# Kernel optimization log

Measured on AMD Instinct MI355X. Metric: run time of the kernel, lower is better.

The kernel has to match this reference:

```python
import jax, jax.numpy as jnp
import numpy as np

PRIMES = (2, 3, 5, 7, 11, 13, 17, 19, 23, 29)
TEMP = 1000.0  # softmax_temperature
B, S = 32, 2048

def _templates(p):
    # circle template for residue r: (cos(2*pi*r/p), sin(2*pi*r/p)) -> [p, 2]
    ang = 2.0 * np.pi * np.arange(p) / p
    return jnp.asarray(np.stack([np.cos(ang), np.sin(ang)], axis=-1).astype(np.float32))

def _mul_onehot(p):
    # onehot[a, b, (a*b) % p] = 1 -> [p, p, p]
    t = (np.arange(p)[:, None] * np.arange(p)[None, :]) % p
    return jnp.asarray((t[..., None] == np.arange(p)).astype(np.float32))

TEMPLATES = [_templates(p) for p in PRIMES]
MUL_OH = [_mul_onehot(p) for p in PRIMES]

def setup_inputs() -> dict:
    key = jax.random.key(0)
    k1, k2 = jax.random.split(key)
    m = len(PRIMES)
    return {
        "a_circle": jax.random.normal(k1, (B, S, m, 2), dtype=jnp.float32),
        "b_circle": jax.random.normal(k2, (B, S, m, 2), dtype=jnp.float32),
    }

def _circle_add(a, b):
    # complex multiply: angles add -> (a + b) mod p on the circle
    ca, sa = a[..., 0], a[..., 1]
    cb, sb = b[..., 0], b[..., 1]
    return jnp.stack([ca * cb - sa * sb, sa * cb + ca * sb], axis=-1)

def _circle_sub(a, b):
    # a - b = a + conj(b): negate sin of b
    b_conj = jnp.stack([b[..., 0], -b[..., 1]], axis=-1)
    return _circle_add(a, b_conj)

def _decode_soft(c_i, tmpl):
    # c_i: [B, S, 2], tmpl: [p, 2] -> soft one-hot over residues [B, S, p]
    sim = jnp.einsum('bsd,pd->bsp', c_i, tmpl)
    return jax.nn.softmax(TEMP * sim, axis=-1)

def _circle_mul(a, b):
    outs = []
    for i, p in enumerate(PRIMES):
        tmpl = TEMPLATES[i]
        a_soft = _decode_soft(a[:, :, i, :], tmpl)
        b_soft = _decode_soft(b[:, :, i, :], tmpl)
        # outer product of soft residues contracted with mul table
        dist = jnp.einsum('bsi,bsj,ijk->bsk', a_soft, b_soft, MUL_OH[i])
        outs.append(dist @ tmpl)  # re-encode to circle: [B, S, 2]
    return jnp.stack(outs, axis=2)  # [B, S, m, 2]

def reference(a_circle, b_circle):
    add = _circle_add(a_circle, b_circle)
    sub = _circle_sub(a_circle, b_circle)
    mul = _circle_mul(a_circle, b_circle)
    return jnp.stack([add, sub, mul], axis=0)  # [3, B, S, m, 2]
```

## Files before the change

### kernel.cpp

```cpp
#include <hip/hip_runtime.h>


#define TEMP_LOG2E 1442.6950408889634f

constexpr double PI_D = 3.14159265358979323846264338327950288;

constexpr double tay_cos(double x) {
    double x2 = x * x, term = 1.0, sum = 1.0;
    for (int k = 1; k <= 15; ++k) { term *= -x2 / double((2 * k - 1) * (2 * k)); sum += term; }
    return sum;
}
constexpr double tay_sin(double x) {
    double x2 = x * x, term = x, sum = x;
    for (int k = 1; k <= 15; ++k) { term *= -x2 / double((2 * k) * (2 * k + 1)); sum += term; }
    return sum;
}
constexpr double ang_red(int r, int P) {
    double x = 2.0 * PI_D * double(r) / double(P);
    return (x > PI_D) ? x - 2.0 * PI_D : x;
}

template <int P> struct TabS { float c[P]; float s[P]; };
template <int P>
constexpr TabS<P> make_tabs() {
    TabS<P> t{};
    for (int r = 0; r < P; ++r) {
        t.c[r] = (float)(double(TEMP_LOG2E) * tay_cos(ang_red(r, P)));
        t.s[r] = (float)(double(TEMP_LOG2E) * tay_sin(ang_red(r, P)));
    }
    return t;
}
template <int P> struct TabE { float c[P / 2 + 1]; float s[P / 2 + 1]; };
template <int P>
constexpr TabE<P> make_tabe() {
    TabE<P> t{};
    for (int k = 0; k <= P / 2; ++k) {
        t.c[k] = (float)tay_cos(ang_red(k, P));
        t.s[k] = (float)tay_sin(ang_red(k, P));
    }
    return t;
}

template <int P>
__device__ __forceinline__ void mul_prime(float ca, float sa, float cb, float sb,
                                          float& oc, float& os) {
    static_assert(P % 2 == 1, "generic path requires odd P");
    constexpr int H = (P - 1) / 2;
    constexpr TabS<P> T = make_tabs<P>();
    constexpr TabE<P> E = make_tabe<P>();

    float ma = -1e30f, mb = -1e30f;
#pragma unroll
    for (int r = 0; r < P; ++r) {
        ma = fmaxf(ma, ca * T.c[r] + sa * T.s[r]);
        mb = fmaxf(mb, cb * T.c[r] + sb * T.s[r]);
    }

    float eb0 = __builtin_amdgcn_exp2f(cb * T.c[0] - mb);
    float Sb = eb0;
    float ub[H], vb[H];
#pragma unroll
    for (int j = 1; j <= H; ++j) {
        float e1 = __builtin_amdgcn_exp2f(cb * T.c[j] + sb * T.s[j] - mb);
        float e2 = __builtin_amdgcn_exp2f(cb * T.c[P - j] + sb * T.s[P - j] - mb);
        Sb += e1 + e2;
        ub[j - 1] = e1 + e2;
        vb[j - 1] = e1 - e2;
    }

    float A[H], Bacc[H];
#pragma unroll
    for (int k = 0; k < H; ++k) { A[k] = 0.f; Bacc[k] = 0.f; }

    float ea0 = __builtin_amdgcn_exp2f(ca * T.c[0] - ma);
    float Sa = ea0;
#pragma unroll
    for (int i = 1; i <= H; ++i) {
        float f1 = __builtin_amdgcn_exp2f(ca * T.c[i] + sa * T.s[i] - ma);
        float f2 = __builtin_amdgcn_exp2f(ca * T.c[P - i] + sa * T.s[P - i] - ma);
        Sa += f1 + f2;
        const float ua = f1 + f2, va = f1 - f2;
#pragma unroll
        for (int j = 1; j <= H; ++j) {
            const int k0 = (i * j) % P;
            const int kr = (k0 <= H) ? k0 : P - k0;
            A[kr - 1] = fmaf(ua, ub[j - 1], A[kr - 1]);
            if (k0 <= H) Bacc[kr - 1] = fmaf(va,  vb[j - 1], Bacc[kr - 1]);
            else         Bacc[kr - 1] = fmaf(-va, vb[j - 1], Bacc[kr - 1]);
        }
    }

    const float W0 = ea0 * Sb + eb0 * (Sa - ea0);

    float accC = W0, accS = 0.f;
#pragma unroll
    for (int k = 1; k <= H; ++k) {
        accC = fmaf(A[k - 1],    E.c[k], accC);
        accS = fmaf(Bacc[k - 1], E.s[k], accS);
    }
    const float inv = 1.0f / (Sa * Sb);
    oc = accC * inv;
    os = accS * inv;
}

template <>
__device__ __forceinline__ void mul_prime<2>(float ca, float sa, float cb, float sb,
                                             float& oc, float& os) {
    const float ka = ca * TEMP_LOG2E, kb = cb * TEMP_LOG2E;
    const float ma = fabsf(ka), mb = fabsf(kb);
    const float ea0 = __builtin_amdgcn_exp2f(ka - ma);
    const float ea1 = __builtin_amdgcn_exp2f(-ka - ma);
    const float eb0 = __builtin_amdgcn_exp2f(kb - mb);
    const float eb1 = __builtin_amdgcn_exp2f(-kb - mb);
    const float Sa = ea0 + ea1, Sb = eb0 + eb1;
    const float W0 = ea0 * Sb + eb0 * Sa - ea0 * eb0;
    const float W1 = ea1 * eb1;
    oc = (W0 - W1) / (Sa * Sb);
    os = 0.f;
}

__global__ __launch_bounds__(640, 2) void arith_kernel(const float* __restrict__ a,
                                                       const float* __restrict__ b,
                                                       float* __restrict__ out,
                                                       int n_pairs) {
    __shared__ float2 t0[64 * 11], t1[64 * 11];
    __shared__ float2 o2[64 * 11];

    const int t = threadIdx.x;
    const int pr = t / 10, of = t - pr * 10;
    const int li = pr * 11 + of;
    const int gf = blockIdx.x * 640 + t;
    const int planef2 = n_pairs * 10;
    float2* o = (float2*)out;

    {
        const float2 av = ((const float2*)a)[gf];
        const float2 bv = ((const float2*)b)[gf];
        t0[li] = av;
        t1[li] = bv;
        const float pcc = av.x * bv.x, pss = av.y * bv.y;
        const float psc = av.y * bv.x, pcs = av.x * bv.y;
        o[gf]           = make_float2(pcc - pss, psc + pcs);
        o[planef2 + gf] = make_float2(pcc + pss, psc - pcs);
    }
    __syncthreads();

    {
        const int lane = t & 63;
        const int pi = t >> 6;
        const int lc = lane * 11 + pi;
        const float2 av = t0[lc];
        const float2 bv = t1[lc];
        float oc, os;
        switch (pi) {
            case 0: mul_prime<2>(av.x, av.y, bv.x, bv.y, oc, os); break;
            case 1: mul_prime<3>(av.x, av.y, bv.x, bv.y, oc, os); break;
            case 2: mul_prime<5>(av.x, av.y, bv.x, bv.y, oc, os); break;
            case 3: mul_prime<7>(av.x, av.y, bv.x, bv.y, oc, os); break;
            case 4: mul_prime<11>(av.x, av.y, bv.x, bv.y, oc, os); break;
            case 5: mul_prime<13>(av.x, av.y, bv.x, bv.y, oc, os); break;
            case 6: mul_prime<17>(av.x, av.y, bv.x, bv.y, oc, os); break;
            case 7: mul_prime<19>(av.x, av.y, bv.x, bv.y, oc, os); break;
            case 8: mul_prime<23>(av.x, av.y, bv.x, bv.y, oc, os); break;
            default: mul_prime<29>(av.x, av.y, bv.x, bv.y, oc, os); break;
        }
        o2[lc] = make_float2(oc, os);
    }
    __syncthreads();

    o[2 * planef2 + gf] = o2[li];
}

extern "C" void kernel_launch(void* const* d_in, const int* in_sizes, int n_in,
                              void* d_out, int out_size, void* d_ws, size_t ws_size,
                              hipStream_t stream) {
    const float* a = (const float*)d_in[0];
    const float* b = (const float*)d_in[1];
    float* out = (float*)d_out;
    const int n_pairs = in_sizes[0] / 20;
    const int n_groups = n_pairs / 64;

    dim3 block(640);
    dim3 grid(n_groups);
    arith_kernel<<<grid, block, 0, stream>>>(a, b, out, n_pairs);
}
```

Measured before the change: 74.34 us.

## Rebalance prime work across waves with 256-thread blocks of 128 rows

Replaces the one-wave-per-prime mapping, where the wave handling p=29 dominated block latency, with 4 waves per block covering 128 rows. Two waves each run primes {29,17,13,2} and the other two run {23,19,11,7,5,3}, which evens out the cost per wave. Loads and add/sub stores now loop 5 times per thread. The intent is to remove the load imbalance caused by the largest-prime wave. In exchange, each thread carries more serialized work and uses more registers, and occupancy may change.

```diff
diff --git a/kernel.cpp b/kernel.cpp
--- a/kernel.cpp
+++ b/kernel.cpp
@@ -119,56 +119,70 @@
     os = 0.f;
 }
 
-__global__ __launch_bounds__(640, 2) void arith_kernel(const float* __restrict__ a,
+__global__ __launch_bounds__(256, 2) void arith_kernel(const float* __restrict__ a,
                                                        const float* __restrict__ b,
                                                        float* __restrict__ out,
                                                        int n_pairs) {
-    __shared__ float2 t0[64 * 11], t1[64 * 11];
-    __shared__ float2 o2[64 * 11];
+    __shared__ float2 ta[128 * 11], tb[128 * 11], om[128 * 11];
 
     const int t = threadIdx.x;
-    const int pr = t / 10, of = t - pr * 10;
-    const int li = pr * 11 + of;
-    const int gf = blockIdx.x * 640 + t;
+    const int gbase = blockIdx.x * 1280;
     const int planef2 = n_pairs * 10;
     float2* o = (float2*)out;
 
-    {
-        const float2 av = ((const float2*)a)[gf];
-        const float2 bv = ((const float2*)b)[gf];
-        t0[li] = av;
-        t1[li] = bv;
+#pragma unroll
+    for (int it = 0; it < 5; ++it) {
+        const int idx = it * 256 + t;
+        const int pr = idx / 10, of = idx - pr * 10;
+        const int sl = pr * 11 + of;
+        const float2 av = ((const float2*)a)[gbase + idx];
+        const float2 bv = ((const float2*)b)[gbase + idx];
+        ta[sl] = av;
+        tb[sl] = bv;
         const float pcc = av.x * bv.x, pss = av.y * bv.y;
         const float psc = av.y * bv.x, pcs = av.x * bv.y;
-        o[gf]           = make_float2(pcc - pss, psc + pcs);
-        o[planef2 + gf] = make_float2(pcc + pss, psc - pcs);
+        o[gbase + idx]            = make_float2(pcc - pss, psc + pcs);
+        o[planef2 + gbase + idx]  = make_float2(pcc + pss, psc - pcs);
     }
     __syncthreads();
 
     {
         const int lane = t & 63;
-        const int pi = t >> 6;
-        const int lc = lane * 11 + pi;
-        const float2 av = t0[lc];
-        const float2 bv = t1[lc];
-        float oc, os;
-        switch (pi) {
-            case 0: mul_prime<2>(av.x, av.y, bv.x, bv.y, oc, os); break;
-            case 1: mul_prime<3>(av.x, av.y, bv.x, bv.y, oc, os); break;
-            case 2: mul_prime<5>(av.x, av.y, bv.x, bv.y, oc, os); break;
-            case 3: mul_prime<7>(av.x, av.y, bv.x, bv.y, oc, os); break;
-            case 4: mul_prime<11>(av.x, av.y, bv.x, bv.y, oc, os); break;
-            case 5: mul_prime<13>(av.x, av.y, bv.x, bv.y, oc, os); break;
-            case 6: mul_prime<17>(av.x, av.y, bv.x, bv.y, oc, os); break;
-            case 7: mul_prime<19>(av.x, av.y, bv.x, bv.y, oc, os); break;
-            case 8: mul_prime<23>(av.x, av.y, bv.x, bv.y, oc, os); break;
-            default: mul_prime<29>(av.x, av.y, bv.x, bv.y, oc, os); break;
+        const int row = ((t >> 6) & 1) * 64 + lane;
+        const int rb = row * 11;
+
+#define DO_PRIME(P, OFI)                                                     \
+        {                                                                    \
+            const float2 av = ta[rb + (OFI)];                                \
+            const float2 bv = tb[rb + (OFI)];                                \
+            float oc, os;                                                    \
+            mul_prime<P>(av.x, av.y, bv.x, bv.y, oc, os);                    \
+            om[rb + (OFI)] = make_float2(oc, os);                            \
         }
-        o2[lc] = make_float2(oc, os);
+
+        if (t < 128) {
+            DO_PRIME(29, 9)
+            DO_PRIME(17, 6)
+            DO_PRIME(13, 5)
+            DO_PRIME(2, 0)
+        } else {
+            DO_PRIME(23, 8)
+            DO_PRIME(19, 7)
+            DO_PRIME(11, 4)
+            DO_PRIME(7, 3)
+            DO_PRIME(5, 2)
+            DO_PRIME(3, 1)
+        }
+#undef DO_PRIME
     }
     __syncthreads();
 
-    o[2 * planef2 + gf] = o2[li];
+#pragma unroll
+    for (int it = 0; it < 5; ++it) {
+        const int idx = it * 256 + t;
+        const int pr = idx / 10, of = idx - pr * 10;
+        o[2 * planef2 + gbase + idx] = om[pr * 11 + of];
+    }
 }
 
 extern "C" void kernel_launch(void* const* d_in, const int* in_sizes, int n_in,
@@ -178,9 +192,9 @@
     const float* b = (const float*)d_in[1];
     float* out = (float*)d_out;
     const int n_pairs = in_sizes[0] / 20;
-    const int n_groups = n_pairs / 64;
-
-    dim3 block(640);
-    dim3 grid(n_groups);
+    const int n_blocks = n_pairs / 128;
+
+    dim3 block(256);
+    dim3 grid(n_blocks);
     arith_kernel<<<grid, block, 0, stream>>>(a, b, out, n_pairs);
 }
```

Result: faster. 69.36 us (-6.7%).
